# Kernel optimization log

Hardware: AMD Instinct MI355X
Metric: run time of the kernel (lower is better)

Reference implementation:

```python
import jax, jax.numpy as jnp
import numpy as np

D_MODEL = 1024
NUM_HEADS = 16
HEAD_DIM = D_MODEL // NUM_HEADS
SCALE = HEAD_DIM ** -0.5
RMS_EPS = 1e-6


def setup_inputs() -> dict:
    key = jax.random.key(0)
    ks = jax.random.split(key, 6)
    B, T, S = 2, 1024, 2048
    return {
        "query": jax.random.normal(ks[0], (B, T, D_MODEL), dtype=jnp.float32),
        "context": jax.random.normal(ks[1], (B, S, D_MODEL), dtype=jnp.float32),
        "Wq": jax.random.normal(ks[2], (D_MODEL, D_MODEL), dtype=jnp.float32) * (D_MODEL ** -0.5),
        "Wk": jax.random.normal(ks[3], (D_MODEL, D_MODEL), dtype=jnp.float32) * (D_MODEL ** -0.5),
        "Wv": jax.random.normal(ks[4], (D_MODEL, D_MODEL), dtype=jnp.float32) * (D_MODEL ** -0.5),
        "Wo": jax.random.normal(ks[5], (D_MODEL, D_MODEL), dtype=jnp.float32) * (D_MODEL ** -0.5),
        "rms_weight": jnp.ones((D_MODEL,), dtype=jnp.float32),
    }


def _alibi_bias(T, S, num_heads, dtype):
    # slopes = 1 / 2**((h+1)/H) for h in 0..H-1
    base = jnp.arange(1, num_heads + 1, dtype=dtype)
    slopes = 1.0 / jnp.power(jnp.asarray(2.0, dtype), base / num_heads)  # [H]
    rel = jnp.abs(jnp.arange(T, dtype=dtype)[:, None] - jnp.arange(S, dtype=dtype)[None, :])  # [T,S]
    return -slopes[None, :, None, None] * rel[None, None, :, :]  # [1,H,T,S]


def _rmsnorm(x, w, eps=RMS_EPS):
    ms = jnp.mean(jnp.square(x), axis=-1, keepdims=True)
    return x * jax.lax.rsqrt(ms + eps) * w


def reference(query, context, Wq, Wk, Wv, Wo, rms_weight):
    B, T, D = query.shape
    S = context.shape[1]
    H, hd = NUM_HEADS, HEAD_DIM
    # projections (torch Linear: x @ W.T), split into heads: [B,H,L,hd]
    q = (query @ Wq.T).reshape(B, T, H, hd).transpose(0, 2, 1, 3)
    k = (context @ Wk.T).reshape(B, S, H, hd).transpose(0, 2, 1, 3)
    v = (context @ Wv.T).reshape(B, S, H, hd).transpose(0, 2, 1, 3)
    bias = _alibi_bias(T, S, H, query.dtype)
    scores = jnp.einsum("bhtd,bhsd->bhts", q, k) * SCALE + bias
    attn = jax.nn.softmax(scores, axis=-1)
    out = jnp.einsum("bhts,bhsd->bhtd", attn, v)  # [B,H,T,hd]
    out = out.transpose(0, 2, 1, 3).reshape(B, T, D) @ Wo.T
    return _rmsnorm(query + out, rms_weight)
```

## Files before the change

### kernel.cpp

```cpp
#include <hip/hip_runtime.h>
#include <cstdint>
#include <cstddef>

#define D_MODEL 1024
#define NHEADS  16
#define HDIM    64
#define BATCH   2
#define TQ      1024
#define SKL     2048
#define BAND    96
#define BANDW   256
#define SUSED   1152

typedef __bf16 bf16x8 __attribute__((ext_vector_type(8)));
typedef float  f32x4  __attribute__((ext_vector_type(4)));

__device__ __forceinline__ unsigned short f2bf(float f) {
  union { float f; unsigned int u; } v; v.f = f;
  unsigned int r = v.u + 0x7FFFu + ((v.u >> 16) & 1u);
  return (unsigned short)(r >> 16);
}

__device__ __forceinline__ void load_lds16(const void* g, void* l) {
  __builtin_amdgcn_global_load_lds(
      (__attribute__((address_space(1))) void*)(uintptr_t)g,
      (__attribute__((address_space(3))) void*)l,
      16, 0, 0);
}

struct CastArgs {
  const float*    src[6];
  unsigned short* dst[6];
  int bstart[6];
};

__global__ __launch_bounds__(256) void cast_kernel(CastArgs a) {
  int bx = blockIdx.x;
  int seg = 0;
#pragma unroll
  for (int i = 1; i < 6; ++i) seg += (bx >= a.bstart[i]) ? 1 : 0;
  size_t idx = (size_t)(bx - a.bstart[seg]) * 1024 + threadIdx.x * 4;
  float4 v = *(const float4*)(a.src[seg] + idx);
  ushort4 o;
  o.x = f2bf(v.x); o.y = f2bf(v.y); o.z = f2bf(v.z); o.w = f2bf(v.w);
  *(ushort4*)(a.dst[seg] + idx) = o;
}

struct ProjArgs {
  const unsigned short* A[3];
  const unsigned short* W[3];
  unsigned short*       C[3];
  int   ytiles[3];
  int   row_mod[3];
  int   row_stride[3];
  float scale[3];
};

__global__ __launch_bounds__(256)
void gemm_proj(ProjArgs pa) {
  const int z = blockIdx.z;
  if ((int)blockIdx.y >= pa.ytiles[z]) return;
  __shared__ unsigned short sA[128 * 32];
  __shared__ unsigned short sB[64 * 32];
  const unsigned short* __restrict__ A = pa.A[z];
  const unsigned short* __restrict__ W = pa.W[z];
  unsigned short* __restrict__ C = pa.C[z];
  const float scale = pa.scale[z];
  const int tid = threadIdx.x, lane = tid & 63, w = tid >> 6;
  const int quad = lane >> 4, l16 = lane & 15;
  const int wm = (w >> 1) * 64, wn = (w & 1) * 32;
  const int bm = blockIdx.y * 128, bn = blockIdx.x * 64;
  const int bb = bm / pa.row_mod[z];
  const int sloc = bm - bb * pa.row_mod[z];
  const size_t arow0 = (size_t)bb * pa.row_stride[z] + sloc;

  f32x4 acc[4][2];
#pragma unroll
  for (int i = 0; i < 4; ++i)
#pragma unroll
    for (int j = 0; j < 2; ++j) acc[i][j] = (f32x4){0.f, 0.f, 0.f, 0.f};

  const int rowS = tid >> 2, kc = tid & 3;
  for (int k0 = 0; k0 < 1024; k0 += 32) {
    __syncthreads();
    load_lds16(A + (arow0 + rowS) * 1024 + k0 + kc * 8,      sA + tid * 8);
    load_lds16(A + (arow0 + rowS + 64) * 1024 + k0 + kc * 8, sA + (tid + 256) * 8);
    load_lds16(W + (size_t)(bn + rowS) * 1024 + k0 + kc * 8, sB + tid * 8);
    __syncthreads();

    bf16x8 af[4], bfr[2];
#pragma unroll
    for (int i = 0; i < 4; ++i)
      af[i] = *(const bf16x8*)(sA + (wm + i * 16 + l16) * 32 + quad * 8);
#pragma unroll
    for (int j = 0; j < 2; ++j)
      bfr[j] = *(const bf16x8*)(sB + (wn + j * 16 + l16) * 32 + quad * 8);
#pragma unroll
    for (int i = 0; i < 4; ++i)
#pragma unroll
      for (int j = 0; j < 2; ++j)
        acc[i][j] = __builtin_amdgcn_mfma_f32_16x16x32_bf16(af[i], bfr[j], acc[i][j], 0, 0, 0);
  }

  if (z == 2) {
#pragma unroll
    for (int i = 0; i < 4; ++i) {
#pragma unroll
      for (int j = 0; j < 2; ++j) {
        int col = bn + wn + j * 16 + l16;
        int s = sloc + wm + i * 16 + quad * 4;
        ushort4 pk;
        pk.x = f2bf(acc[i][j][0]);
        pk.y = f2bf(acc[i][j][1]);
        pk.z = f2bf(acc[i][j][2]);
        pk.w = f2bf(acc[i][j][3]);
        *(ushort4*)(C + ((size_t)bb * 1024 + col) * SKL + s) = pk;
      }
    }
  } else {
#pragma unroll
    for (int i = 0; i < 4; ++i)
#pragma unroll
      for (int j = 0; j < 2; ++j)
#pragma unroll
        for (int r = 0; r < 4; ++r)
          C[(arow0 + wm + i * 16 + quad * 4 + r) * 1024 + bn + wn + j * 16 + l16] =
              f2bf(acc[i][j][r] * scale);
  }
}

__global__ __launch_bounds__(256)
void gemm_out(const unsigned short* __restrict__ A,
              const unsigned short* __restrict__ W,
              float* __restrict__ Cbase) {
  __shared__ unsigned short sA[128 * 32];
  __shared__ unsigned short sB[64 * 32];
  const int tid = threadIdx.x, lane = tid & 63, w = tid >> 6;
  const int quad = lane >> 4, l16 = lane & 15;
  const int wm = (w >> 1) * 64, wn = (w & 1) * 32;
  const size_t bm = (size_t)blockIdx.y * 128;
  const size_t bn = (size_t)blockIdx.x * 64;
  const int z = blockIdx.z;
  float* __restrict__ C = Cbase + (size_t)z * TQ * BATCH * 1024;

  f32x4 acc[4][2];
#pragma unroll
  for (int i = 0; i < 4; ++i)
#pragma unroll
    for (int j = 0; j < 2; ++j) acc[i][j] = (f32x4){0.f, 0.f, 0.f, 0.f};

  const int rowS = tid >> 2, kc = tid & 3;
  const int kbeg = z * 512, kend = kbeg + 512;
  for (int k0 = kbeg; k0 < kend; k0 += 32) {
    __syncthreads();
    load_lds16(A + (bm + rowS) * 1024 + k0 + kc * 8,      sA + tid * 8);
    load_lds16(A + (bm + rowS + 64) * 1024 + k0 + kc * 8, sA + (tid + 256) * 8);
    load_lds16(W + (bn + rowS) * 1024 + k0 + kc * 8,      sB + tid * 8);
    __syncthreads();

    bf16x8 af[4], bfr[2];
#pragma unroll
    for (int i = 0; i < 4; ++i)
      af[i] = *(const bf16x8*)(sA + (wm + i * 16 + l16) * 32 + quad * 8);
#pragma unroll
    for (int j = 0; j < 2; ++j)
      bfr[j] = *(const bf16x8*)(sB + (wn + j * 16 + l16) * 32 + quad * 8);
#pragma unroll
    for (int i = 0; i < 4; ++i)
#pragma unroll
      for (int j = 0; j < 2; ++j)
        acc[i][j] = __builtin_amdgcn_mfma_f32_16x16x32_bf16(af[i], bfr[j], acc[i][j], 0, 0, 0);
  }

#pragma unroll
  for (int i = 0; i < 4; ++i)
#pragma unroll
    for (int j = 0; j < 2; ++j)
#pragma unroll
      for (int r = 0; r < 4; ++r)
        C[(bm + wm + i * 16 + quad * 4 + r) * 1024 + bn + wn + j * 16 + l16] = acc[i][j][r];
}

#define PTS 72
#define VCH (BANDW / 8)
__global__ __launch_bounds__(256)
void attn_kernel(const unsigned short* __restrict__ Q,
                 const unsigned short* __restrict__ K,
                 const unsigned short* __restrict__ Vt,
                 unsigned short* __restrict__ O) {
  __shared__ unsigned short sK[BANDW * 64];
  __shared__ unsigned short sV[64 * BANDW];
  __shared__ unsigned short sP[4][16 * PTS];

  const int tid = threadIdx.x, lane = tid & 63, w = tid >> 6;
  const int quad = lane >> 4, l16 = lane & 15;
  const int bh = blockIdx.y, b = bh >> 4, h = bh & 15;
  const int q0b = blockIdx.x * 64;
  const int q0 = q0b + w * 16;

  const int s_lo = (q0b >= BAND) ? (q0b - BAND) : 0;

  const unsigned short* qrow = Q + (size_t)(b * TQ + q0 + l16) * D_MODEL + h * HDIM;
  bf16x8 qa0 = *(const bf16x8*)(qrow + quad * 8);
  bf16x8 qa1 = *(const bf16x8*)(qrow + 32 + quad * 8);

  const unsigned short* Kbase = K + (size_t)(b * SKL + s_lo) * D_MODEL + h * HDIM;
  const unsigned short* Vbase = Vt + (size_t)bh * HDIM * SKL + s_lo;

#pragma unroll
  for (int it = 0; it < 8; ++it) {
    int flat = it * 256 + tid;
    int row = flat >> 3;
    int kc = (flat & 7) ^ (row & 7);
    load_lds16(Kbase + (size_t)row * D_MODEL + kc * 8, sK + flat * 8);
  }
#pragma unroll
  for (int it = 0; it < 8; ++it) {
    int flat = it * 256 + tid;
    int d = flat >> 5;
    int c = flat & 31;
    int cs = c ^ (d & 7);
    load_lds16(Vbase + (size_t)d * SKL + cs * 8, sV + flat * 8);
  }
  __syncthreads();

  float l_lane[4] = {0.f, 0.f, 0.f, 0.f};
  f32x4 o_acc[4];
#pragma unroll
  for (int j = 0; j < 4; ++j) o_acc[j] = (f32x4){0.f, 0.f, 0.f, 0.f};
  const float slope = exp2f(-(float)(h + 1) * (1.0f / NHEADS));
  unsigned short* pw = sP[w];

  for (int s0 = 0; s0 < BANDW; s0 += 64) {
    f32x4 sc[4];
#pragma unroll
    for (int n = 0; n < 4; ++n) {
      int srow = s0 + n * 16 + l16;
      int sw = srow & 7;
      bf16x8 kb0 = *(const bf16x8*)(sK + (srow * 8 + (quad ^ sw)) * 8);
      bf16x8 kb1 = *(const bf16x8*)(sK + (srow * 8 + ((4 + quad) ^ sw)) * 8);
      f32x4 zz = (f32x4){0.f, 0.f, 0.f, 0.f};
      zz = __builtin_amdgcn_mfma_f32_16x16x32_bf16(qa0, kb0, zz, 0, 0, 0);
      zz = __builtin_amdgcn_mfma_f32_16x16x32_bf16(qa1, kb1, zz, 0, 0, 0);
      sc[n] = zz;
    }

#pragma unroll
    for (int r = 0; r < 4; ++r) {
      float tpos = (float)(q0 + quad * 4 + r);
#pragma unroll
      for (int n = 0; n < 4; ++n) {
        float spos = (float)(s_lo + s0 + n * 16 + l16);
        float p = __expf(fmaf(-slope, fabsf(tpos - spos), sc[n][r]) - 24.0f);
        sc[n][r] = p;
        l_lane[r] += p;
      }
    }

#pragma unroll
    for (int n = 0; n < 4; ++n)
#pragma unroll
      for (int r = 0; r < 4; ++r)
        pw[(quad * 4 + r) * PTS + n * 16 + l16] = f2bf(sc[n][r]);
    __asm__ volatile("s_waitcnt lgkmcnt(0)" ::: "memory");

    bf16x8 pa0 = *(const bf16x8*)(pw + l16 * PTS + quad * 8);
    bf16x8 pa1 = *(const bf16x8*)(pw + l16 * PTS + 32 + quad * 8);
#pragma unroll
    for (int j = 0; j < 4; ++j) {
      int drow = j * 16 + l16;
      int dw = drow & 7;
      int rb = drow * VCH + (s0 >> 3);
      bf16x8 vb0 = *(const bf16x8*)(sV + (rb + (quad ^ dw)) * 8);
      bf16x8 vb1 = *(const bf16x8*)(sV + (rb + ((4 + quad) ^ dw)) * 8);
      o_acc[j] = __builtin_amdgcn_mfma_f32_16x16x32_bf16(pa0, vb0, o_acc[j], 0, 0, 0);
      o_acc[j] = __builtin_amdgcn_mfma_f32_16x16x32_bf16(pa1, vb1, o_acc[j], 0, 0, 0);
    }
  }

#pragma unroll
  for (int r = 0; r < 4; ++r) {
    float ls = l_lane[r];
    ls += __shfl_xor(ls, 1);
    ls += __shfl_xor(ls, 2);
    ls += __shfl_xor(ls, 4);
    ls += __shfl_xor(ls, 8);
    l_lane[r] = 1.0f / ls;
  }
#pragma unroll
  for (int j = 0; j < 4; ++j)
#pragma unroll
    for (int r = 0; r < 4; ++r)
      O[(size_t)(b * TQ + q0 + quad * 4 + r) * D_MODEL + h * HDIM + j * 16 + l16] =
          f2bf(o_acc[j][r] * l_lane[r]);
}

__global__ __launch_bounds__(256)
void rmsnorm_kernel(const float* __restrict__ q, const float* __restrict__ p0,
                    const float* __restrict__ p1, const float* __restrict__ w,
                    float* __restrict__ out) {
  const int row = blockIdx.x, tid = threadIdx.x;
  float4 a  = ((const float4*)(q  + (size_t)row * 1024))[tid];
  float4 b0 = ((const float4*)(p0 + (size_t)row * 1024))[tid];
  float4 b1 = ((const float4*)(p1 + (size_t)row * 1024))[tid];
  float4 y = {a.x + b0.x + b1.x, a.y + b0.y + b1.y, a.z + b0.z + b1.z, a.w + b0.w + b1.w};
  float ss = y.x * y.x + y.y * y.y + y.z * y.z + y.w * y.w;
#pragma unroll
  for (int m = 1; m < 64; m <<= 1) ss += __shfl_xor(ss, m);
  __shared__ float sred[4];
  if ((tid & 63) == 0) sred[tid >> 6] = ss;
  __syncthreads();
  float tot = sred[0] + sred[1] + sred[2] + sred[3];
  float rs = rsqrtf(tot * (1.0f / 1024.0f) + 1e-6f);
  float4 wv = ((const float4*)w)[tid];
  float4 o = {y.x * rs * wv.x, y.y * rs * wv.y, y.z * rs * wv.z, y.w * rs * wv.w};
  ((float4*)(out + (size_t)row * 1024))[tid] = o;
}

extern "C" void kernel_launch(void* const* d_in, const int* in_sizes, int n_in,
                              void* d_out, int out_size, void* d_ws, size_t ws_size,
                              hipStream_t stream) {
  (void)in_sizes; (void)n_in; (void)out_size; (void)ws_size;
  const float* query   = (const float*)d_in[0];
  const float* context = (const float*)d_in[1];
  const float* Wq      = (const float*)d_in[2];
  const float* Wk      = (const float*)d_in[3];
  const float* Wv      = (const float*)d_in[4];
  const float* Wo      = (const float*)d_in[5];
  const float* rmsw    = (const float*)d_in[6];

  char* ws = (char*)d_ws;
  unsigned short* qb    = (unsigned short*)(ws + 0);
  unsigned short* cb    = (unsigned short*)(ws + 4194304);
  unsigned short* wqb   = (unsigned short*)(ws + 12582912);
  unsigned short* wkb   = (unsigned short*)(ws + 14680064);
  unsigned short* wvb   = (unsigned short*)(ws + 16777216);
  unsigned short* wob   = (unsigned short*)(ws + 18874368);
  unsigned short* Qp    = (unsigned short*)(ws + 20971520);
  unsigned short* Kp    = (unsigned short*)(ws + 25165824);
  unsigned short* Vt    = (unsigned short*)(ws + 33554432);
  unsigned short* attnb = (unsigned short*)(ws + 41943040);
  float*          proj  = (float*)(ws + 46137344);

  CastArgs ca;
  ca.src[0] = query;   ca.dst[0] = qb;
  ca.src[1] = context; ca.dst[1] = cb;
  ca.src[2] = Wq;      ca.dst[2] = wqb;
  ca.src[3] = Wk;      ca.dst[3] = wkb;
  ca.src[4] = Wv;      ca.dst[4] = wvb;
  ca.src[5] = Wo;      ca.dst[5] = wob;
  ca.bstart[0] = 0;    ca.bstart[1] = 2048; ca.bstart[2] = 6144;
  ca.bstart[3] = 7168; ca.bstart[4] = 8192; ca.bstart[5] = 9216;
  cast_kernel<<<10240, 256, 0, stream>>>(ca);

  ProjArgs pa;
  pa.A[0] = qb; pa.W[0] = wqb; pa.C[0] = Qp;
  pa.ytiles[0] = TQ * BATCH / 128;
  pa.row_mod[0] = TQ * BATCH; pa.row_stride[0] = TQ * BATCH; pa.scale[0] = 0.125f;
  pa.A[1] = cb; pa.W[1] = wkb; pa.C[1] = Kp;
  pa.ytiles[1] = SUSED * BATCH / 128;
  pa.row_mod[1] = SUSED; pa.row_stride[1] = SKL; pa.scale[1] = 1.0f;
  pa.A[2] = cb; pa.W[2] = wvb; pa.C[2] = Vt;
  pa.ytiles[2] = SUSED * BATCH / 128;
  pa.row_mod[2] = SUSED; pa.row_stride[2] = SKL; pa.scale[2] = 1.0f;
  gemm_proj<<<dim3(16, 18, 3), 256, 0, stream>>>(pa);

  attn_kernel<<<dim3(16, 32), 256, 0, stream>>>(Qp, Kp, Vt, attnb);
  gemm_out<<<dim3(16, 16, 2), 256, 0, stream>>>(attnb, wob, proj);
  rmsnorm_kernel<<<2048, 256, 0, stream>>>(query, proj, proj + (size_t)TQ * BATCH * 1024,
                                           rmsw, (float*)d_out);
}
```

Before: 153.7 us.

## Fuse K and V projections sharing context tiles; cast only used context rows

The K and V projections now run in the same block, so each context tile loaded into LDS feeds both the Wk and Wv MFMAs. This halves context reads for those projections and drops the separate z-slice. The cast kernel now converts only the first SUSED context rows per batch, skipping rows the attention band never touches. In exchange, the fused blocks hold twice the accumulators, so register pressure rises and fewer blocks may fit per CU.

```diff
diff --git a/kernel.cpp b/kernel.cpp
--- a/kernel.cpp
+++ b/kernel.cpp
@@ -29,16 +29,16 @@
 }
 
 struct CastArgs {
-  const float*    src[6];
-  unsigned short* dst[6];
-  int bstart[6];
+  const float*    src[7];
+  unsigned short* dst[7];
+  int bstart[7];
 };
 
 __global__ __launch_bounds__(256) void cast_kernel(CastArgs a) {
   int bx = blockIdx.x;
   int seg = 0;
 #pragma unroll
-  for (int i = 1; i < 6; ++i) seg += (bx >= a.bstart[i]) ? 1 : 0;
+  for (int i = 1; i < 7; ++i) seg += (bx >= a.bstart[i]) ? 1 : 0;
   size_t idx = (size_t)(bx - a.bstart[seg]) * 1024 + threadIdx.x * 4;
   float4 v = *(const float4*)(a.src[seg] + idx);
   ushort4 o;
@@ -47,85 +47,133 @@
 }
 
 struct ProjArgs {
-  const unsigned short* A[3];
-  const unsigned short* W[3];
-  unsigned short*       C[3];
-  int   ytiles[3];
-  int   row_mod[3];
-  int   row_stride[3];
-  float scale[3];
+  const unsigned short* Aq;
+  const unsigned short* Wq;
+  const unsigned short* Ac;
+  const unsigned short* Wk;
+  const unsigned short* Wv;
+  unsigned short*       Qp;
+  unsigned short*       Kp;
+  unsigned short*       Vt;
 };
 
 __global__ __launch_bounds__(256)
 void gemm_proj(ProjArgs pa) {
-  const int z = blockIdx.z;
-  if ((int)blockIdx.y >= pa.ytiles[z]) return;
   __shared__ unsigned short sA[128 * 32];
-  __shared__ unsigned short sB[64 * 32];
-  const unsigned short* __restrict__ A = pa.A[z];
-  const unsigned short* __restrict__ W = pa.W[z];
-  unsigned short* __restrict__ C = pa.C[z];
-  const float scale = pa.scale[z];
+  __shared__ unsigned short sB0[64 * 32];
+  __shared__ unsigned short sB1[64 * 32];
   const int tid = threadIdx.x, lane = tid & 63, w = tid >> 6;
   const int quad = lane >> 4, l16 = lane & 15;
   const int wm = (w >> 1) * 64, wn = (w & 1) * 32;
-  const int bm = blockIdx.y * 128, bn = blockIdx.x * 64;
-  const int bb = bm / pa.row_mod[z];
-  const int sloc = bm - bb * pa.row_mod[z];
-  const size_t arow0 = (size_t)bb * pa.row_stride[z] + sloc;
-
-  f32x4 acc[4][2];
-#pragma unroll
-  for (int i = 0; i < 4; ++i)
-#pragma unroll
-    for (int j = 0; j < 2; ++j) acc[i][j] = (f32x4){0.f, 0.f, 0.f, 0.f};
-
+  const int bn = blockIdx.x * 64;
   const int rowS = tid >> 2, kc = tid & 3;
-  for (int k0 = 0; k0 < 1024; k0 += 32) {
-    __syncthreads();
-    load_lds16(A + (arow0 + rowS) * 1024 + k0 + kc * 8,      sA + tid * 8);
-    load_lds16(A + (arow0 + rowS + 64) * 1024 + k0 + kc * 8, sA + (tid + 256) * 8);
-    load_lds16(W + (size_t)(bn + rowS) * 1024 + k0 + kc * 8, sB + tid * 8);
-    __syncthreads();
-
-    bf16x8 af[4], bfr[2];
-#pragma unroll
-    for (int i = 0; i < 4; ++i)
-      af[i] = *(const bf16x8*)(sA + (wm + i * 16 + l16) * 32 + quad * 8);
-#pragma unroll
-    for (int j = 0; j < 2; ++j)
-      bfr[j] = *(const bf16x8*)(sB + (wn + j * 16 + l16) * 32 + quad * 8);
-#pragma unroll
-    for (int i = 0; i < 4; ++i)
+
+  if (blockIdx.z == 0) {
+    if ((int)blockIdx.y >= 16) return;
+    const int bm = blockIdx.y * 128;
+    const unsigned short* __restrict__ A = pa.Aq;
+    const unsigned short* __restrict__ W = pa.Wq;
+
+    f32x4 acc[4][2];
+#pragma unroll
+    for (int i = 0; i < 4; ++i)
+#pragma unroll
+      for (int j = 0; j < 2; ++j) acc[i][j] = (f32x4){0.f, 0.f, 0.f, 0.f};
+
+    for (int k0 = 0; k0 < 1024; k0 += 32) {
+      __syncthreads();
+      load_lds16(A + (size_t)(bm + rowS) * 1024 + k0 + kc * 8,      sA + tid * 8);
+      load_lds16(A + (size_t)(bm + rowS + 64) * 1024 + k0 + kc * 8, sA + (tid + 256) * 8);
+      load_lds16(W + (size_t)(bn + rowS) * 1024 + k0 + kc * 8,      sB0 + tid * 8);
+      __syncthreads();
+
+      bf16x8 af[4], bfr[2];
+#pragma unroll
+      for (int i = 0; i < 4; ++i)
+        af[i] = *(const bf16x8*)(sA + (wm + i * 16 + l16) * 32 + quad * 8);
 #pragma unroll
       for (int j = 0; j < 2; ++j)
-        acc[i][j] = __builtin_amdgcn_mfma_f32_16x16x32_bf16(af[i], bfr[j], acc[i][j], 0, 0, 0);
-  }
-
-  if (z == 2) {
-#pragma unroll
-    for (int i = 0; i < 4; ++i) {
+        bfr[j] = *(const bf16x8*)(sB0 + (wn + j * 16 + l16) * 32 + quad * 8);
+#pragma unroll
+      for (int i = 0; i < 4; ++i)
+#pragma unroll
+        for (int j = 0; j < 2; ++j)
+          acc[i][j] = __builtin_amdgcn_mfma_f32_16x16x32_bf16(af[i], bfr[j], acc[i][j], 0, 0, 0);
+    }
+
+#pragma unroll
+    for (int i = 0; i < 4; ++i)
+#pragma unroll
+      for (int j = 0; j < 2; ++j)
+#pragma unroll
+        for (int r = 0; r < 4; ++r)
+          pa.Qp[(size_t)(bm + wm + i * 16 + quad * 4 + r) * 1024 + bn + wn + j * 16 + l16] =
+              f2bf(acc[i][j][r] * 0.125f);
+  } else {
+    const int bm = blockIdx.y * 128;
+    const int bb = bm / SUSED;
+    const int sloc = bm - bb * SUSED;
+    const size_t arow0 = (size_t)bb * SKL + sloc;
+    const unsigned short* __restrict__ A  = pa.Ac;
+    const unsigned short* __restrict__ Wk = pa.Wk;
+    const unsigned short* __restrict__ Wv = pa.Wv;
+
+    f32x4 acck[4][2], accv[4][2];
+#pragma unroll
+    for (int i = 0; i < 4; ++i)
+#pragma unroll
+      for (int j = 0; j < 2; ++j) {
+        acck[i][j] = (f32x4){0.f, 0.f, 0.f, 0.f};
+        accv[i][j] = (f32x4){0.f, 0.f, 0.f, 0.f};
+      }
+
+    for (int k0 = 0; k0 < 1024; k0 += 32) {
+      __syncthreads();
+      load_lds16(A + (arow0 + rowS) * 1024 + k0 + kc * 8,       sA + tid * 8);
+      load_lds16(A + (arow0 + rowS + 64) * 1024 + k0 + kc * 8,  sA + (tid + 256) * 8);
+      load_lds16(Wk + (size_t)(bn + rowS) * 1024 + k0 + kc * 8, sB0 + tid * 8);
+      load_lds16(Wv + (size_t)(bn + rowS) * 1024 + k0 + kc * 8, sB1 + tid * 8);
+      __syncthreads();
+
+      bf16x8 af[4], bk[2], bv[2];
+#pragma unroll
+      for (int i = 0; i < 4; ++i)
+        af[i] = *(const bf16x8*)(sA + (wm + i * 16 + l16) * 32 + quad * 8);
+#pragma unroll
+      for (int j = 0; j < 2; ++j) {
+        bk[j] = *(const bf16x8*)(sB0 + (wn + j * 16 + l16) * 32 + quad * 8);
+        bv[j] = *(const bf16x8*)(sB1 + (wn + j * 16 + l16) * 32 + quad * 8);
+      }
+#pragma unroll
+      for (int i = 0; i < 4; ++i)
+#pragma unroll
+        for (int j = 0; j < 2; ++j) {
+          acck[i][j] = __builtin_amdgcn_mfma_f32_16x16x32_bf16(af[i], bk[j], acck[i][j], 0, 0, 0);
+          accv[i][j] = __builtin_amdgcn_mfma_f32_16x16x32_bf16(af[i], bv[j], accv[i][j], 0, 0, 0);
+        }
+    }
+
+#pragma unroll
+    for (int i = 0; i < 4; ++i)
+#pragma unroll
+      for (int j = 0; j < 2; ++j)
+#pragma unroll
+        for (int r = 0; r < 4; ++r)
+          pa.Kp[(arow0 + wm + i * 16 + quad * 4 + r) * 1024 + bn + wn + j * 16 + l16] =
+              f2bf(acck[i][j][r]);
+#pragma unroll
+    for (int i = 0; i < 4; ++i)
 #pragma unroll
       for (int j = 0; j < 2; ++j) {
         int col = bn + wn + j * 16 + l16;
         int s = sloc + wm + i * 16 + quad * 4;
         ushort4 pk;
-        pk.x = f2bf(acc[i][j][0]);
-        pk.y = f2bf(acc[i][j][1]);
-        pk.z = f2bf(acc[i][j][2]);
-        pk.w = f2bf(acc[i][j][3]);
-        *(ushort4*)(C + ((size_t)bb * 1024 + col) * SKL + s) = pk;
+        pk.x = f2bf(accv[i][j][0]);
+        pk.y = f2bf(accv[i][j][1]);
+        pk.z = f2bf(accv[i][j][2]);
+        pk.w = f2bf(accv[i][j][3]);
+        *(ushort4*)(pa.Vt + ((size_t)bb * 1024 + col) * SKL + s) = pk;
       }
-    }
-  } else {
-#pragma unroll
-    for (int i = 0; i < 4; ++i)
-#pragma unroll
-      for (int j = 0; j < 2; ++j)
-#pragma unroll
-        for (int r = 0; r < 4; ++r)
-          C[(arow0 + wm + i * 16 + quad * 4 + r) * 1024 + bn + wn + j * 16 + l16] =
-              f2bf(acc[i][j][r] * scale);
   }
 }
 
@@ -343,27 +391,23 @@
   float*          proj  = (float*)(ws + 46137344);
 
   CastArgs ca;
-  ca.src[0] = query;   ca.dst[0] = qb;
-  ca.src[1] = context; ca.dst[1] = cb;
-  ca.src[2] = Wq;      ca.dst[2] = wqb;
-  ca.src[3] = Wk;      ca.dst[3] = wkb;
-  ca.src[4] = Wv;      ca.dst[4] = wvb;
-  ca.src[5] = Wo;      ca.dst[5] = wob;
-  ca.bstart[0] = 0;    ca.bstart[1] = 2048; ca.bstart[2] = 6144;
-  ca.bstart[3] = 7168; ca.bstart[4] = 8192; ca.bstart[5] = 9216;
-  cast_kernel<<<10240, 256, 0, stream>>>(ca);
+  ca.src[0] = query;                   ca.dst[0] = qb;
+  ca.src[1] = context;                 ca.dst[1] = cb;
+  ca.src[2] = context + 2048 * 1024;   ca.dst[2] = cb + 2048 * 1024;
+  ca.src[3] = Wq;                      ca.dst[3] = wqb;
+  ca.src[4] = Wk;                      ca.dst[4] = wkb;
+  ca.src[5] = Wv;                      ca.dst[5] = wvb;
+  ca.src[6] = Wo;                      ca.dst[6] = wob;
+  ca.bstart[0] = 0;    ca.bstart[1] = 2048; ca.bstart[2] = 3200;
+  ca.bstart[3] = 4352; ca.bstart[4] = 5376; ca.bstart[5] = 6400;
+  ca.bstart[6] = 7424;
+  cast_kernel<<<8448, 256, 0, stream>>>(ca);
 
   ProjArgs pa;
-  pa.A[0] = qb; pa.W[0] = wqb; pa.C[0] = Qp;
-  pa.ytiles[0] = TQ * BATCH / 128;
-  pa.row_mod[0] = TQ * BATCH; pa.row_stride[0] = TQ * BATCH; pa.scale[0] = 0.125f;
-  pa.A[1] = cb; pa.W[1] = wkb; pa.C[1] = Kp;
-  pa.ytiles[1] = SUSED * BATCH / 128;
-  pa.row_mod[1] = SUSED; pa.row_stride[1] = SKL; pa.scale[1] = 1.0f;
-  pa.A[2] = cb; pa.W[2] = wvb; pa.C[2] = Vt;
-  pa.ytiles[2] = SUSED * BATCH / 128;
-  pa.row_mod[2] = SUSED; pa.row_stride[2] = SKL; pa.scale[2] = 1.0f;
-  gemm_proj<<<dim3(16, 18, 3), 256, 0, stream>>>(pa);
+  pa.Aq = qb;  pa.Wq = wqb; pa.Qp = Qp;
+  pa.Ac = cb;  pa.Wk = wkb; pa.Wv = wvb;
+  pa.Kp = Kp;  pa.Vt = Vt;
+  gemm_proj<<<dim3(16, 18, 2), 256, 0, stream>>>(pa);
 
   attn_kernel<<<dim3(16, 32), 256, 0, stream>>>(Qp, Kp, Vt, attnb);
   gemm_out<<<dim3(16, 16, 2), 256, 0, stream>>>(attnb, wob, proj);
```

Result: no change. 153.0 us (-0.5%).
